# Optimization experiments

Measured on AMD Instinct MI355X. Metric: run time of the kernel, lower is better.

The kernel has to match this reference:

```python
import jax, jax.numpy as jnp
import numpy as np
from jax import lax

# 8 neighbor offsets of the Moore neighborhood (matches neighbors_roll_axes)
OFFS = [(i, j) for i in range(-1, 2) for j in range(-1, 2) if not (i == 0 and j == 0)]


def _neighbors(g):
    # g: [B,1,H,W]; toroidal shifts
    return [jnp.roll(g, (i, j), axis=(2, 3)) for i, j in OFFS]


def _binary_step(gb):
    # Conway rule on boolean grid: alive if sum==3 or (alive and sum==2)
    s = sum(n.astype(jnp.int32) for n in _neighbors(gb))
    return (s == 3) | (gb & (s == 2))


def _prob_step(p):
    # P(next alive) = P(exactly 3 of 8 neighbors alive) + P(exactly 2 alive) * p
    # Computed via a count-distribution DP over the 8 independent Bernoulli
    # neighbors -- mathematically identical to the C(8,2)+C(8,3)=84 enumerated
    # products in the torch code, but O(8) fused elementwise passes.
    z = jnp.zeros_like(p)
    c0, c1, c2, c3 = jnp.ones_like(p), z, z, z  # P(count==k); >=4 absorbed
    for q in _neighbors(p):
        c3 = c3 * (1 - q) + c2 * q
        c2 = c2 * (1 - q) + c1 * q
        c1 = c1 * (1 - q) + c0 * q
        c0 = c0 * (1 - q)
    return c3 + c2 * p


def _cconv(x, w, b, pad):
    # circular ('wrap') padding conv, NCHW/OIHW
    if pad:
        x = jnp.pad(x, ((0, 0), (0, 0), (pad, pad), (pad, pad)), mode='wrap')
    y = lax.conv_general_dilated(x, w, (1, 1), 'VALID',
                                 dimension_numbers=('NCHW', 'OIHW', 'NCHW'))
    return y + b[None, :, None, None]


def _block(x, xp, params):
    w1, b1, w2, b2, w3, b3, w4, b4 = params
    # stencil features computed under no_grad in the original
    xp_bin = lax.stop_gradient(xp > 0.5)
    x_pred_bin = _binary_step(xp_bin)
    x_pred = lax.stop_gradient(_prob_step(lax.stop_gradient(xp)))
    h = jnp.concatenate([x, xp, xp_bin.astype(x.dtype), x_pred,
                         x_pred_bin.astype(x.dtype)], axis=1)  # [B,5,H,W]
    h = jax.nn.relu(_cconv(h, w1, b1, 2))
    h = jax.nn.relu(_cconv(h, w2, b2, 1))
    h = jax.nn.relu(_cconv(h, w3, b3, 0))
    return jax.nn.sigmoid(_cconv(h, w4, b4, 1))


def setup_inputs() -> dict:
    key = jax.random.key(0)
    ks = jax.random.split(key, 6)
    B, H, W = 4, 256, 256
    x = jax.random.uniform(ks[0], (B, 1, H, W), jnp.float32)

    def wi(k, shape):
        fan_in = shape[1] * shape[2] * shape[3]
        return (jax.random.normal(k, shape, jnp.float32) / np.sqrt(fan_in)).astype(jnp.float32)

    w1 = wi(ks[1], (256, 5, 5, 5));   b1 = jnp.zeros((256,), jnp.float32)
    w2 = wi(ks[2], (256, 256, 3, 3)); b2 = jnp.zeros((256,), jnp.float32)
    w3 = wi(ks[3], (256, 256, 1, 1)); b3 = jnp.zeros((256,), jnp.float32)
    w4 = wi(ks[4], (1, 256, 3, 3));   b4 = jnp.zeros((1,), jnp.float32)
    return {"x": x, "w1": w1, "b1": b1, "w2": w2, "b2": b2,
            "w3": w3, "b3": b3, "w4": w4, "b4": b4, "n_it": 5}


def reference(x, w1, b1, w2, b2, w3, b3, w4, b4, n_it):
    params = (w1, b1, w2, b2, w3, b3, w4, b4)
    xp = x
    for _ in range(n_it):
        xp = _block(x, xp, params)
    return xp
```

## Files before the change

### kernel.cpp

```cpp
#include <hip/hip_runtime.h>
#include <hip/hip_bf16.h>


#define NPIX (4 * 256 * 256)

typedef double v4d __attribute__((ext_vector_type(4)));

__global__ __launch_bounds__(64) void probe_mode(int* __restrict__ modep)
{
    int lr = threadIdx.x & 15;
    v4d p1 = {}, p2 = {};
    p1 = __builtin_amdgcn_mfma_f64_16x16x4f64((double)lr, 1.0, p1, 0, 0, 0);
    p2 = __builtin_amdgcn_mfma_f64_16x16x4f64(1.0, (double)lr, p2, 0, 0, 0);
    double v1 = __shfl(p1[0], 16);
    double v2 = __shfl(p2[0], 16);
    if (threadIdx.x == 0)
        *modep = (v1 == 16.0) ? 0 : (v1 == 4.0) ? 1 : (v2 == 16.0) ? 2 : 3;
}

__global__ __launch_bounds__(256) void xinit_kernel(
    const float* __restrict__ x, double* __restrict__ xp64)
{
    int p = blockIdx.x * 256 + threadIdx.x;
    xp64[p] = (double)x[p];
}

__global__ __launch_bounds__(256) void stencil_strip(
    const float* __restrict__ x, const double* __restrict__ xp,
    double* __restrict__ h0, size_t h0_is,
    int job0, int ns_shift, int R)
{
    int slot = blockIdx.y;
    int j = job0 + slot;
    int img = j >> ns_shift;
    int r0 = (j & ((1 << ns_shift) - 1)) * R;
    int pbase = img << 16;
    int y = (r0 - 4 + blockIdx.x) & 255;
    int col = threadIdx.x;
    double q[8];
    int s = 0, idx = 0;
    #pragma unroll
    for (int i = -1; i <= 1; ++i)
        #pragma unroll
        for (int jj = -1; jj <= 1; ++jj) {
            if (i == 0 && jj == 0) continue;
            int ys = (y - i) & 255, xs = (col - jj) & 255;
            double v = xp[pbase + ((ys << 8) | xs)];
            q[idx++] = v;
            s += (v > 0.5) ? 1 : 0;
        }
    double c = xp[pbase + ((y << 8) | col)];
    bool alive = c > 0.5;
    bool binnext = (s == 3) || (alive && s == 2);
    double c0 = 1.0, c1 = 0.0, c2 = 0.0, c3 = 0.0;
    #pragma unroll
    for (int k = 0; k < 8; ++k) {
        double qq = q[k], r = 1.0 - qq;
        c3 = c3 * r + c2 * qq;
        c2 = c2 * r + c1 * qq;
        c1 = c1 * r + c0 * qq;
        c0 = c0 * r;
    }
    double xpred = c3 + c2 * c;
    double* o = h0 + slot * h0_is + ((size_t)blockIdx.x * 256 + col) * 8;
    o[0] = (double)x[pbase + ((y << 8) | col)];
    o[1] = c;
    o[2] = alive ? 1.0 : 0.0;
    o[3] = xpred;
    o[4] = binnext ? 1.0 : 0.0;
    o[5] = 0.0; o[6] = 0.0; o[7] = 0.0;
}

template<int CIN, int TK, int KH, int KW>
__global__ __launch_bounds__(512, 6) void conv_gemm(
    const double* __restrict__ A, size_t a_is,
    const double* __restrict__ Wp,
    const float* __restrict__ bias,
    double* __restrict__ O, size_t o_is,
    int delta, const int* __restrict__ modep)
{
    constexpr int PW = KW / 2, PH = KH / 2;
    constexpr int CHUNKS = CIN / TK;
    constexpr int NCH = KH * KW * CHUNKS;
    constexpr int LPP = TK / 2;
    constexpr int NA = 128 * LPP;
    constexpr int NW = TK * 32;
    constexpr int NT = NA + NW;
    constexpr int TPT = (NT + 511) / 512;

    __shared__ double Asmem[2][TK][130];
    __shared__ double Wsmem[2][TK][66];

    const double* Ai = A + blockIdx.z * a_is;
    double* Oi = O + blockIdx.z * o_is;
    const int mode = *modep;

    const int tid = threadIdx.x;
    const int pm0 = blockIdx.x * 128;
    const int on0 = blockIdx.y * 64;
    const int yl0 = pm0 >> 8;
    const int c0l = pm0 & 255;
    const int wave = tid >> 6, lane = tid & 63;
    const int lq = lane >> 4, lr = lane & 15;
    const int wr = (wave >> 1) * 32;
    const int wc = (wave & 1) * 32;

    v4d acc[2][2] = {};
    double2 st[TPT];

    auto load_tasks = [&](int ch) {
        int tap = ch / CHUNKS, cc = ch - tap * CHUNKS;
        int dy = tap / KW - PH, dx = tap % KW - PW;
        int c0 = cc * TK;
        int kglob = tap * CIN + c0;
        int srow = yl0 + dy + delta;
        #pragma unroll
        for (int i = 0; i < TPT; ++i) {
            int u = tid + i * 512;
            if (NT % 512 == 0 || u < NT) {
                if (u < NA) {
                    int px = u / LPP, pp = u % LPP;
                    int xs = (c0l + px + dx) & 255;
                    st[i] = *(const double2*)(
                        Ai + (size_t)((srow << 8) | xs) * CIN + c0 + pp * 2);
                } else {
                    int u2 = u - NA;
                    int row = u2 >> 5, cp = (u2 & 31) << 1;
                    st[i] = *(const double2*)&Wp[
                        (size_t)(kglob + row) * 256 + on0 + cp];
                }
            }
        }
    };
    auto write_tasks = [&](int buf) {
        #pragma unroll
        for (int i = 0; i < TPT; ++i) {
            int u = tid + i * 512;
            if (NT % 512 == 0 || u < NT) {
                if (u < NA) {
                    int px = u / LPP, pp = u % LPP;
                    Asmem[buf][pp * 2 + 0][px] = st[i].x;
                    Asmem[buf][pp * 2 + 1][px] = st[i].y;
                } else {
                    int u2 = u - NA;
                    int row = u2 >> 5, cp = (u2 & 31) << 1;
                    *(double2*)&Wsmem[buf][row][cp] = st[i];
                }
            }
        }
    };

    load_tasks(0);
    write_tasks(0);
    __syncthreads();
    for (int ch = 0; ch < NCH; ++ch) {
        const int cur = ch & 1;
        if (ch + 1 < NCH) load_tasks(ch + 1);
        __builtin_amdgcn_s_setprio(1);
        #pragma unroll
        for (int k0 = 0; k0 < TK / 4; ++k0) {
            const int kk = k0 * 4 + lq;
            double a[2], b[2];
            a[0] = Asmem[cur][kk][wr + lr];
            a[1] = Asmem[cur][kk][wr + 16 + lr];
            b[0] = Wsmem[cur][kk][wc + lr];
            b[1] = Wsmem[cur][kk][wc + 16 + lr];
            #pragma unroll
            for (int rt = 0; rt < 2; ++rt)
                #pragma unroll
                for (int ct = 0; ct < 2; ++ct)
                    acc[rt][ct] = __builtin_amdgcn_mfma_f64_16x16x4f64(
                        a[rt], b[ct], acc[rt][ct], 0, 0, 0);
        }
        __builtin_amdgcn_s_setprio(0);
        if (ch + 1 < NCH) write_tasks(cur ^ 1);
        __syncthreads();
    }

    #pragma unroll
    for (int rt = 0; rt < 2; ++rt)
        #pragma unroll
        for (int ct = 0; ct < 2; ++ct)
            #pragma unroll
            for (int i = 0; i < 4; ++i) {
                int hq = lq * 4 + i, hi = i * 4 + lq;
                int rl = (mode == 0) ? hq : (mode == 1) ? hi : lr;
                int cl = (mode <= 1) ? lr : (mode == 2) ? hq : hi;
                int px = pm0 + wr + rt * 16 + rl;
                int oc = on0 + wc + ct * 16 + cl;
                Oi[(size_t)px * 256 + oc] =
                    fmax(acc[rt][ct][i] + (double)bias[oc], 0.0);
            }
}

__global__ __launch_bounds__(512, 6) void conv2_gemm(
    const double* __restrict__ A, size_t a_is,
    const double* __restrict__ Wp,
    const float* __restrict__ bias,
    double* __restrict__ O, size_t o_is,
    const int* __restrict__ modep)
{
    __shared__ double Asmem[2][8][130];
    __shared__ double Wsmem[2][24][66];
    constexpr int NA = 520;
    constexpr int NT = 1288;

    const double* Ai = A + blockIdx.z * a_is;
    double* Oi = O + blockIdx.z * o_is;
    const int mode = *modep;

    const int tid = threadIdx.x;
    const int pm0 = blockIdx.x * 128;
    const int on0 = blockIdx.y * 64;
    const int yrow = pm0 >> 8;
    const int col0 = pm0 & 255;
    const int wave = tid >> 6, lane = tid & 63;
    const int lq = lane >> 4, lr = lane & 15;
    const int wr = (wave >> 1) * 32;
    const int wc = (wave & 1) * 32;

    v4d acc[2][2] = {};
    double2 st[3];

    auto load_tasks = [&](int ch) {
        int dy = ch >> 5;
        int cc = ch & 31;
        int c0 = cc * 8;
        int srow = yrow + dy;
        #pragma unroll
        for (int i = 0; i < 3; ++i) {
            int u = tid + i * 512;
            if (u < NT) {
                if (u < NA) {
                    int px = u >> 2, pp = u & 3;
                    int xs = (col0 - 1 + px) & 255;
                    st[i] = *(const double2*)(
                        Ai + (size_t)((srow << 8) | xs) * 256 + c0 + pp * 2);
                } else {
                    int u2 = u - NA;
                    int row = u2 >> 5, cp = (u2 & 31) << 1;
                    int tap = dy * 3 + (row >> 3);
                    int k = tap * 256 + c0 + (row & 7);
                    st[i] = *(const double2*)&Wp[(size_t)k * 256 + on0 + cp];
                }
            }
        }
    };
    auto write_tasks = [&](int buf) {
        #pragma unroll
        for (int i = 0; i < 3; ++i) {
            int u = tid + i * 512;
            if (u < NT) {
                if (u < NA) {
                    int px = u >> 2, pp = u & 3;
                    Asmem[buf][pp * 2 + 0][px] = st[i].x;
                    Asmem[buf][pp * 2 + 1][px] = st[i].y;
                } else {
                    int u2 = u - NA;
                    int row = u2 >> 5, cp = (u2 & 31) << 1;
                    *(double2*)&Wsmem[buf][row][cp] = st[i];
                }
            }
        }
    };

    load_tasks(0);
    write_tasks(0);
    __syncthreads();
    for (int ch = 0; ch < 96; ++ch) {
        const int cur = ch & 1;
        if (ch + 1 < 96) load_tasks(ch + 1);
        __builtin_amdgcn_s_setprio(1);
        #pragma unroll
        for (int dx = 0; dx < 3; ++dx)
            #pragma unroll
            for (int k0 = 0; k0 < 2; ++k0) {
                const int kA = k0 * 4 + lq;
                const int kW = dx * 8 + k0 * 4 + lq;
                double a[2], b[2];
                a[0] = Asmem[cur][kA][dx + wr + lr];
                a[1] = Asmem[cur][kA][dx + wr + 16 + lr];
                b[0] = Wsmem[cur][kW][wc + lr];
                b[1] = Wsmem[cur][kW][wc + 16 + lr];
                #pragma unroll
                for (int rt = 0; rt < 2; ++rt)
                    #pragma unroll
                    for (int ct = 0; ct < 2; ++ct)
                        acc[rt][ct] = __builtin_amdgcn_mfma_f64_16x16x4f64(
                            a[rt], b[ct], acc[rt][ct], 0, 0, 0);
            }
        __builtin_amdgcn_s_setprio(0);
        if (ch + 1 < 96) write_tasks(cur ^ 1);
        __syncthreads();
    }

    #pragma unroll
    for (int rt = 0; rt < 2; ++rt)
        #pragma unroll
        for (int ct = 0; ct < 2; ++ct)
            #pragma unroll
            for (int i = 0; i < 4; ++i) {
                int hq = lq * 4 + i, hi = i * 4 + lq;
                int rl = (mode == 0) ? hq : (mode == 1) ? hi : lr;
                int cl = (mode <= 1) ? lr : (mode == 2) ? hq : hi;
                int px = pm0 + wr + rt * 16 + rl;
                int oc = on0 + wc + ct * 16 + cl;
                Oi[(size_t)px * 256 + oc] =
                    fmax(acc[rt][ct][i] + (double)bias[oc], 0.0);
            }
}

__global__ __launch_bounds__(256) void conv4_sig(
    const double* __restrict__ H3, size_t h3_is,
    const float* __restrict__ w4, const float* __restrict__ b4,
    float* __restrict__ out, double* __restrict__ xp_new,
    int job0, int ns_shift, int R)
{
    __shared__ double w4s[2304];
    int tid = threadIdx.x;
    for (int i = tid; i < 2304; i += 256) w4s[i] = (double)w4[i];
    __syncthreads();
    int slot = blockIdx.y;
    int j = job0 + slot;
    int img = j >> ns_shift;
    int r0 = (j & ((1 << ns_shift) - 1)) * R;
    const double* H3i = H3 + slot * h3_is;
    int pbase = img << 16;
    int lane = tid & 63, wv = tid >> 6;
    int p0 = blockIdx.x * 64 + wv * 16;
    for (int pi = 0; pi < 16; ++pi) {
        int pl = p0 + pi;
        int yl = pl >> 8, col = pl & 255;
        double acc = 0.0;
        #pragma unroll
        for (int tap = 0; tap < 9; ++tap) {
            int row = yl + tap / 3 - 1 + 1;
            int xs = (col + tap % 3 - 1) & 255;
            const double* src = H3i + (size_t)((row << 8) | xs) * 256;
            #pragma unroll
            for (int jj = 0; jj < 4; ++jj) {
                int c = lane + 64 * jj;
                acc = fma(src[c], w4s[c * 9 + tap], acc);
            }
        }
        #pragma unroll
        for (int off = 32; off; off >>= 1) acc += __shfl_xor(acc, off, 64);
        if (lane == 0) {
            double v = acc + (double)b4[0];
            double s = 1.0 / (1.0 + exp(-v));
            int p = pbase + (((r0 + yl) << 8) | col);
            out[p] = (float)s;
            xp_new[p] = s;
        }
    }
}

__global__ void repack_w1(const float* __restrict__ w1, double* __restrict__ W1p) {
    int t = blockIdx.x * 256 + threadIdx.x;
    if (t >= 25 * 8 * 256) return;
    int oc = t & 255, cin = (t >> 8) & 7, tap = t >> 11;
    W1p[t] = (cin < 5) ? (double)w1[oc * 125 + cin * 25 + tap] : 0.0;
}
__global__ void repack_w2(const float* __restrict__ w2, double* __restrict__ W2p) {
    int t = blockIdx.x * 256 + threadIdx.x;
    if (t >= 9 * 256 * 256) return;
    int oc = t & 255, cin = (t >> 8) & 255, tap = t >> 16;
    W2p[t] = (double)w2[((oc << 8) | cin) * 9 + tap];
}
__global__ void repack_w3(const float* __restrict__ w3, double* __restrict__ W3p) {
    int t = blockIdx.x * 256 + threadIdx.x;
    if (t >= 256 * 256) return;
    int oc = t & 255, cin = t >> 8;
    W3p[t] = (double)w3[oc * 256 + cin];
}

extern "C" void kernel_launch(void* const* d_in, const int* in_sizes, int n_in,
                              void* d_out, int out_size, void* d_ws, size_t ws_size,
                              hipStream_t stream)
{
    const float* x  = (const float*)d_in[0];
    const float* w1 = (const float*)d_in[1];
    const float* b1 = (const float*)d_in[2];
    const float* w2 = (const float*)d_in[3];
    const float* b2 = (const float*)d_in[4];
    const float* w3 = (const float*)d_in[5];
    const float* b3 = (const float*)d_in[6];
    const float* w4 = (const float*)d_in[7];
    const float* b4 = (const float*)d_in[8];
    float* out = (float*)d_out;

    char* ws = (char*)d_ws;
    double* W1p = (double*)(ws);
    double* W2p = (double*)(ws + 409600ull);
    double* W3p = (double*)(ws + 5128192ull);
    double* xpA = (double*)(ws + 5652480ull);
    double* xpB = (double*)(ws + 7749632ull);
    int*   modep = (int*)(ws + 9846784ull);
    char*  bufs = ws + 9847040ull;
    const size_t base_need = 9847040ull;
    const size_t ROWD  = 524288ull;
    const size_t ROWH0 = 16384ull;

    const int cand_r[14] = {64, 128, 256, 64, 32, 64, 16, 32, 16, 8, 8, 4, 4, 2};
    const int cand_g[14] = { 4,   2,   1,  3,  4,  2,  4,  2,  2, 4, 2, 2, 1, 1};
    int R = 2, G = 1;
    for (int ci = 0; ci < 14; ++ci) {
        int r = cand_r[ci], g = cand_g[ci];
        size_t need = base_need + (size_t)g *
            ((size_t)(r + 8) * ROWH0 + (size_t)(2 * r + 6) * ROWD);
        if (ws_size >= need) { R = r; G = g; break; }
    }
    int ns_shift = 0;
    while ((256 >> ns_shift) != R) ++ns_shift;
    const int NSTRIP = 256 / R;
    const int jobs = 4 * NSTRIP;

    double* h0 = (double*)bufs;
    double* h1 = (double*)(bufs + (size_t)G * (R + 8) * ROWH0);
    double* h2 = (double*)((char*)h1 + (size_t)G * (R + 4) * ROWD);
    double* h3 = h1;
    const size_t h0_is = (size_t)(R + 8) * 256 * 8;
    const size_t h1_is = (size_t)(R + 4) * 256 * 256;
    const size_t h2_is = (size_t)(R + 2) * 256 * 256;

    probe_mode<<<1, 64, 0, stream>>>(modep);
    repack_w1<<<200, 256, 0, stream>>>(w1, W1p);
    repack_w2<<<2304, 256, 0, stream>>>(w2, W2p);
    repack_w3<<<256, 256, 0, stream>>>(w3, W3p);
    xinit_kernel<<<NPIX / 256, 256, 0, stream>>>(x, xpA);

    for (int it = 0; it < 5; ++it) {
        const double* xp_rd = (it & 1) ? xpB : xpA;
        double*       xp_wr = (it & 1) ? xpA : xpB;
        for (int j0 = 0; j0 < jobs; j0 += G) {
            int g = (jobs - j0 < G) ? (jobs - j0) : G;
            stencil_strip<<<dim3(R + 8, g), 256, 0, stream>>>(
                x, xp_rd, h0, h0_is, j0, ns_shift, R);
            conv_gemm<8, 8, 5, 5><<<dim3((R + 4) * 2, 4, g), 512, 0, stream>>>(
                h0, h0_is, W1p, b1, h1, h1_is, 2, modep);
            conv2_gemm<<<dim3((R + 2) * 2, 4, g), 512, 0, stream>>>(
                h1, h1_is, W2p, b2, h2, h2_is, modep);
            conv_gemm<256, 16, 1, 1><<<dim3((R + 2) * 2, 4, g), 512, 0, stream>>>(
                h2, h2_is, W3p, b3, h3, h1_is, 0, modep);
            conv4_sig<<<dim3(R * 4, g), 256, 0, stream>>>(
                h3, h1_is, w4, b4, out, xp_wr, j0, ns_shift, R);
        }
    }
}
```

Measured before the change: 42.05 ms.

## Deepen conv GEMM prefetch with dual staging registers and lightweight barriers

Both conv GEMM kernels now unroll the chunk loop by two and use two staging register sets. Each chunk's global loads are issued one phase earlier, and its LDS writes happen before the MFMA work on the other buffer. A custom barrier waits only on LDS counters, not vector-memory counters, so global loads can stay in flight across barriers and latency is hidden better. The cost is doubled staging registers under a tight launch-bounds occupancy target, which risks spills or lower occupancy.

New measurement: 55.56 ms. 32.1% more time.

```diff
diff --git a/kernel.cpp b/kernel.cpp
--- a/kernel.cpp
+++ b/kernel.cpp
@@ -5,6 +5,12 @@
 #define NPIX (4 * 256 * 256)
 
 typedef double v4d __attribute__((ext_vector_type(4)));
+
+#define PIPE_BARRIER() do {                                   \
+    asm volatile("s_waitcnt lgkmcnt(0)" ::: "memory");        \
+    __builtin_amdgcn_s_barrier();                             \
+    __builtin_amdgcn_sched_barrier(0);                        \
+} while (0)
 
 __global__ __launch_bounds__(64) void probe_mode(int* __restrict__ modep)
 {
@@ -106,9 +112,9 @@
     const int wc = (wave & 1) * 32;
 
     v4d acc[2][2] = {};
-    double2 st[TPT];
-
-    auto load_tasks = [&](int ch) {
+    double2 stA[TPT], stB[TPT];
+
+    auto load_tasks = [&](int ch, double2 (&st)[TPT]) {
         int tap = ch / CHUNKS, cc = ch - tap * CHUNKS;
         int dy = tap / KW - PH, dx = tap % KW - PW;
         int c0 = cc * TK;
@@ -132,7 +138,7 @@
             }
         }
     };
-    auto write_tasks = [&](int buf) {
+    auto write_tasks = [&](int buf, double2 (&st)[TPT]) {
         #pragma unroll
         for (int i = 0; i < TPT; ++i) {
             int u = tid + i * 512;
@@ -149,13 +155,7 @@
             }
         }
     };
-
-    load_tasks(0);
-    write_tasks(0);
-    __syncthreads();
-    for (int ch = 0; ch < NCH; ++ch) {
-        const int cur = ch & 1;
-        if (ch + 1 < NCH) load_tasks(ch + 1);
+    auto mfma_step = [&](int cur) {
         __builtin_amdgcn_s_setprio(1);
         #pragma unroll
         for (int k0 = 0; k0 < TK / 4; ++k0) {
@@ -173,8 +173,26 @@
                         a[rt], b[ct], acc[rt][ct], 0, 0, 0);
         }
         __builtin_amdgcn_s_setprio(0);
-        if (ch + 1 < NCH) write_tasks(cur ^ 1);
-        __syncthreads();
+    };
+
+    load_tasks(0, stA);
+    write_tasks(0, stA);
+    load_tasks(1, stB);
+    PIPE_BARRIER();
+
+    for (int ch = 0; ch < NCH; ch += 2) {
+        {
+            if (ch + 1 < NCH) write_tasks(1, stB);
+            mfma_step(0);
+            if (ch + 2 < NCH) load_tasks(ch + 2, stA);
+            PIPE_BARRIER();
+        }
+        if (ch + 1 < NCH) {
+            if (ch + 2 < NCH) write_tasks(0, stA);
+            mfma_step(1);
+            if (ch + 3 < NCH) load_tasks(ch + 3, stB);
+            PIPE_BARRIER();
+        }
     }
 
     #pragma unroll
@@ -204,6 +222,8 @@
     __shared__ double Wsmem[2][24][66];
     constexpr int NA = 520;
     constexpr int NT = 1288;
+    constexpr int TPT = 3;
+    constexpr int NCH = 96;
 
     const double* Ai = A + blockIdx.z * a_is;
     double* Oi = O + blockIdx.z * o_is;
@@ -220,15 +240,15 @@
     const int wc = (wave & 1) * 32;
 
     v4d acc[2][2] = {};
-    double2 st[3];
-
-    auto load_tasks = [&](int ch) {
+    double2 stA[TPT], stB[TPT];
+
+    auto load_tasks = [&](int ch, double2 (&st)[TPT]) {
         int dy = ch >> 5;
         int cc = ch & 31;
         int c0 = cc * 8;
         int srow = yrow + dy;
         #pragma unroll
-        for (int i = 0; i < 3; ++i) {
+        for (int i = 0; i < TPT; ++i) {
             int u = tid + i * 512;
             if (u < NT) {
                 if (u < NA) {
@@ -246,9 +266,9 @@
             }
         }
     };
-    auto write_tasks = [&](int buf) {
-        #pragma unroll
-        for (int i = 0; i < 3; ++i) {
+    auto write_tasks = [&](int buf, double2 (&st)[TPT]) {
+        #pragma unroll
+        for (int i = 0; i < TPT; ++i) {
             int u = tid + i * 512;
             if (u < NT) {
                 if (u < NA) {
@@ -263,13 +283,7 @@
             }
         }
     };
-
-    load_tasks(0);
-    write_tasks(0);
-    __syncthreads();
-    for (int ch = 0; ch < 96; ++ch) {
-        const int cur = ch & 1;
-        if (ch + 1 < 96) load_tasks(ch + 1);
+    auto mfma_step = [&](int cur) {
         __builtin_amdgcn_s_setprio(1);
         #pragma unroll
         for (int dx = 0; dx < 3; ++dx)
@@ -290,8 +304,26 @@
                             a[rt], b[ct], acc[rt][ct], 0, 0, 0);
             }
         __builtin_amdgcn_s_setprio(0);
-        if (ch + 1 < 96) write_tasks(cur ^ 1);
-        __syncthreads();
+    };
+
+    load_tasks(0, stA);
+    write_tasks(0, stA);
+    load_tasks(1, stB);
+    PIPE_BARRIER();
+
+    for (int ch = 0; ch < NCH; ch += 2) {
+        {
+            if (ch + 1 < NCH) write_tasks(1, stB);
+            mfma_step(0);
+            if (ch + 2 < NCH) load_tasks(ch + 2, stA);
+            PIPE_BARRIER();
+        }
+        {
+            if (ch + 2 < NCH) write_tasks(0, stA);
+            mfma_step(1);
+            if (ch + 3 < NCH) load_tasks(ch + 3, stB);
+            PIPE_BARRIER();
+        }
     }
 
     #pragma unroll
```
